# Optimization experiments

Measured on AMD Instinct MI355X. Metric: run time of the kernel, lower is better.

## Reference

```python
import jax, jax.numpy as jnp
import numpy as np

B, N, D = 2, 256, 512
H = 4 * D  # mlp_hidden_dim


def setup_inputs() -> dict:
    key = jax.random.key(0)
    ks = jax.random.split(key, 14)
    s_in = 1.0 / np.sqrt(D)
    s_h = 1.0 / np.sqrt(H)
    s_cat = 1.0 / np.sqrt(2 * D)
    return {
        "x_v": jax.random.normal(ks[0], (B, N, D), jnp.float32),
        "x_a": jax.random.normal(ks[1], (B, N, D), jnp.float32),
        # weights stored as (in, out); y = x @ W + b (same math as torch Linear)
        "W1v": jax.random.uniform(ks[2], (D, H), jnp.float32, -s_in, s_in),
        "b1v": jax.random.uniform(ks[3], (H,), jnp.float32, -s_in, s_in),
        "W1a": jax.random.uniform(ks[4], (D, H), jnp.float32, -s_in, s_in),
        "b1a": jax.random.uniform(ks[5], (H,), jnp.float32, -s_in, s_in),
        "Wmv": jax.random.uniform(ks[6], (H, D), jnp.float32, -s_h, s_h),
        "bmv": jax.random.uniform(ks[7], (D,), jnp.float32, -s_h, s_h),
        "Wma": jax.random.uniform(ks[8], (H, D), jnp.float32, -s_h, s_h),
        "bma": jax.random.uniform(ks[9], (D,), jnp.float32, -s_h, s_h),
        "Wout": jax.random.uniform(ks[10], (2 * D, D), jnp.float32, -s_cat, s_cat),
        "bout": jax.random.uniform(ks[11], (D,), jnp.float32, -s_cat, s_cat),
    }


def reference(x_v, x_a, W1v, b1v, W1a, b1a, Wmv, bmv, Wma, bma, Wout, bout):
    # pairwise Manhattan distance: [B, N, M]
    dist = jnp.sum(jnp.abs(x_v[:, :, None, :] - x_a[:, None, :, :]), axis=-1)
    dv = dist.mean(axis=2)  # [B, N] mean distance of each v-token to all a-tokens
    da = dist.mean(axis=1)  # [B, M]
    xv_w = x_v * dv[..., None]
    xa_w = x_a * da[..., None]
    # dropout prob = 0.0 -> identity
    hv = jax.nn.gelu(xv_w @ W1v + b1v, approximate=False) @ Wmv + bmv
    ha = jax.nn.gelu(xa_w @ W1a + b1a, approximate=False) @ Wma + bma
    combined = jnp.concatenate([hv, ha], axis=-1)  # [B, N, 2D]
    return combined @ Wout + bout
```

## Files before the change

kernel.cpp:

```cpp
#include <hip/hip_runtime.h>
#include <math.h>

#define Bsz  2
#define Ntok 256
#define Ddim 512
#define Hdim 2048
#define Mrows 512

typedef __bf16 bf16_8 __attribute__((ext_vector_type(8)));
typedef __bf16 bf16_4 __attribute__((ext_vector_type(4)));
typedef __bf16 bf16_2 __attribute__((ext_vector_type(2)));
typedef float  f32x4_t __attribute__((ext_vector_type(4)));

struct PrepPtrs {
    const float* src[3];
    __bf16*      dst[3];
    const float* xv;
    const float* xa;
    __bf16*      xbf[2];
    float*       pv;
    float*       pa;
    const float* bm[2];
    const float* Wout;
    const float* bout;
    float*       bc;
    float*       outz;
};

__global__ __launch_bounds__(256) void prep_kernel(PrepPtrs p) {
    __shared__ float tile[64][65];
    __shared__ float red[4][4];

    int blk = blockIdx.x;
    int tid = threadIdx.x;

    if (blk < 640) {
        const int Ks[3]  = {512, 512, 1024};
        const int Ns[3]  = {2048, 2048, 512};
        const int off[4] = {0, 256, 512, 640};
        int mi = 0;
        while (blk >= off[mi + 1]) ++mi;
        int local = blk - off[mi];
        int shift = (mi < 2) ? 5 : 3;
        int bx = local & ((1 << shift) - 1);
        int by = local >> shift;
        const float* src = p.src[mi];
        __bf16*      dst = p.dst[mi];
        int K = Ks[mi], N = Ns[mi];
        int n0 = bx << 6, k0 = by << 6;

        int klb = tid >> 4, nl = (tid & 15) << 2;
#pragma unroll
        for (int pass = 0; pass < 4; ++pass) {
            int kl = (pass << 4) + klb;
            float4 v = *(const float4*)&src[(size_t)(k0 + kl) * N + n0 + nl];
            tile[kl][nl + 0] = v.x;
            tile[kl][nl + 1] = v.y;
            tile[kl][nl + 2] = v.z;
            tile[kl][nl + 3] = v.w;
        }
        __syncthreads();
        int nl2 = tid >> 2, kb = (tid & 3) << 2;
#pragma unroll
        for (int pass = 0; pass < 4; ++pass) {
            int kl2 = (pass << 4) + kb;
            bf16_4 o;
#pragma unroll
            for (int i = 0; i < 4; ++i) o[i] = (__bf16)tile[kl2 + i][nl2];
            *(bf16_4*)&dst[(size_t)(n0 + nl2) * K + k0 + kl2] = o;
        }
    } else if (blk < 1664) {
        int bx   = blk - 640;
        int jc   = bx & 3;
        int g    = bx >> 2;
        int role = g >> 7;
        int b    = (g >> 6) & 1;
        int i0   = (g & 63) << 2;
        const float* Q    = role ? p.xa : p.xv;
        const float* S    = role ? p.xv : p.xa;
        float*       outp = role ? p.pa : p.pv;

        int d0 = tid << 1;
        const float* Qb = Q + ((size_t)b * Ntok + i0) * Ddim + d0;
        const float* Sb = S + ((size_t)b * Ntok + (jc << 6)) * Ddim + d0;

        float2 q[4];
#pragma unroll
        for (int r = 0; r < 4; ++r) q[r] = *(const float2*)(Qb + r * Ddim);

        if (jc == 0) {
            __bf16* xb = p.xbf[role];
#pragma unroll
            for (int r = 0; r < 4; ++r) {
                bf16_2 o;
                o[0] = (__bf16)q[r].x;
                o[1] = (__bf16)q[r].y;
                *(bf16_2*)&xb[((size_t)b * Ntok + i0 + r) * Ddim + d0] = o;
            }
        }

        float acc[4] = {0.f, 0.f, 0.f, 0.f};
#pragma unroll 4
        for (int j = 0; j < 64; ++j) {
            float2 s = *(const float2*)(Sb + (size_t)j * Ddim);
#pragma unroll
            for (int r = 0; r < 4; ++r)
                acc[r] += fabsf(q[r].x - s.x) + fabsf(q[r].y - s.y);
        }
        int lane = tid & 63, wv = tid >> 6;
#pragma unroll
        for (int r = 0; r < 4; ++r) {
            float v = acc[r];
#pragma unroll
            for (int off2 = 32; off2; off2 >>= 1) v += __shfl_down(v, off2);
            if (lane == 0) red[wv][r] = v;
        }
        __syncthreads();
        if (tid < 4) {
            float v = red[0][tid] + red[1][tid] + red[2][tid] + red[3][tid];
            outp[jc * Mrows + b * Ntok + i0 + tid] = v;
        }
    } else if (blk < 1672) {
        int kb = blk - 1664;
        float a0 = 0.f, a1 = 0.f, a2 = 0.f, a3 = 0.f;
#pragma unroll 4
        for (int kk = 0; kk < 128; kk += 2) {
            int k0 = (kb << 7) + kk, k1 = k0 + 1;
            float bk0 = (k0 < 512) ? p.bm[0][k0] : p.bm[1][k0 - 512];
            float bk1 = (k1 < 512) ? p.bm[0][k1] : p.bm[1][k1 - 512];
            a0 += bk0 * p.Wout[(size_t)k0 * Ddim + tid];
            a1 += bk0 * p.Wout[(size_t)k0 * Ddim + tid + 256];
            a2 += bk1 * p.Wout[(size_t)k1 * Ddim + tid];
            a3 += bk1 * p.Wout[(size_t)k1 * Ddim + tid + 256];
        }
        if (kb == 0) { a0 += p.bout[tid]; a1 += p.bout[tid + 256]; }
        p.bc[(kb << 9) + tid]       = a0 + a2;
        p.bc[(kb << 9) + tid + 256] = a1 + a3;
    } else {
        int ib = blk - 1672;
        float4 z4 = {0.f, 0.f, 0.f, 0.f};
        float4* o = (float4*)p.outz + (size_t)ib * 1024 + tid;
#pragma unroll
        for (int pass = 0; pass < 4; ++pass) o[pass * 256] = z4;
    }
}

template <int GELU, int AMODE, int BFP32, int OUTM>
__device__ void gemm_tile(__bf16 (&As)[2][64][40], __bf16 (&Bs)[2][128][40],
                          const void* Aa, int lda, const void* Bv, int ldb,
                          const float* bias, const float* scale4,
                          void* C, int ldc, int Kdim,
                          int m0, int n0, int addBias) {
    const int tid = threadIdx.x;
    const int arow = tid >> 2;
    const int akc  = (tid & 3) << 3;
    const int brow = tid >> 1;
    const int bkc  = (tid & 1) << 4;

    const __bf16* Ab = (const __bf16*)Aa + (size_t)(m0 + arow) * lda + akc;
    const float*  Af = (const float*) Aa + (size_t)(m0 + arow) * lda + akc;
    const __bf16* Bb = (const __bf16*)Bv + (size_t)(n0 + brow) * ldb + bkc;
    const float*  Bf = (const float*) Bv + (size_t)(n0 + brow) * ldb + bkc;

    float s = 1.0f;
    if (AMODE == 1 || AMODE == 3) {
        int m = m0 + arow;
        s = (scale4[m] + scale4[Mrows + m] + scale4[2 * Mrows + m] +
             scale4[3 * Mrows + m]) * (1.0f / 256.0f);
    }

    const int wave = tid >> 6, lane = tid & 63;
    const int moff = (wave >> 1) << 5;
    const int noff = (wave & 1) << 6;
    const int lrow = lane & 15, quad = lane >> 4;

    struct Stage {
        float4 aF0, aF1;
        float4 bF0, bF1, bF2, bF3;
        bf16_8 a8;
        bf16_8 b8a, b8b;
    };
    Stage sR, sN;

    auto loadStage = [&](int kt, Stage& st) {
        if (BFP32) {
            st.bF0 = *(const float4*)(Bf + kt);
            st.bF1 = *(const float4*)(Bf + kt + 4);
            st.bF2 = *(const float4*)(Bf + kt + 8);
            st.bF3 = *(const float4*)(Bf + kt + 12);
        } else {
            st.b8a = *(const bf16_8*)(Bb + kt);
            st.b8b = *(const bf16_8*)(Bb + kt + 8);
        }
        if (AMODE == 1) {
            st.aF0 = *(const float4*)(Af + kt);
            st.aF1 = *(const float4*)(Af + kt + 4);
        } else {
            st.a8 = *(const bf16_8*)(Ab + kt);
        }
    };
    auto storeStage = [&](int buf, const Stage& st) {
        bf16_8 a8;
        if (AMODE == 1) {
            a8[0] = (__bf16)(st.aF0.x * s); a8[1] = (__bf16)(st.aF0.y * s);
            a8[2] = (__bf16)(st.aF0.z * s); a8[3] = (__bf16)(st.aF0.w * s);
            a8[4] = (__bf16)(st.aF1.x * s); a8[5] = (__bf16)(st.aF1.y * s);
            a8[6] = (__bf16)(st.aF1.z * s); a8[7] = (__bf16)(st.aF1.w * s);
        } else if (AMODE == 3) {
#pragma unroll
            for (int i = 0; i < 8; ++i)
                a8[i] = (__bf16)((float)st.a8[i] * s);
        } else {
            a8 = st.a8;
        }
        bf16_8 b8a, b8b;
        if (BFP32) {
            b8a[0] = (__bf16)st.bF0.x; b8a[1] = (__bf16)st.bF0.y;
            b8a[2] = (__bf16)st.bF0.z; b8a[3] = (__bf16)st.bF0.w;
            b8a[4] = (__bf16)st.bF1.x; b8a[5] = (__bf16)st.bF1.y;
            b8a[6] = (__bf16)st.bF1.z; b8a[7] = (__bf16)st.bF1.w;
            b8b[0] = (__bf16)st.bF2.x; b8b[1] = (__bf16)st.bF2.y;
            b8b[2] = (__bf16)st.bF2.z; b8b[3] = (__bf16)st.bF2.w;
            b8b[4] = (__bf16)st.bF3.x; b8b[5] = (__bf16)st.bF3.y;
            b8b[6] = (__bf16)st.bF3.z; b8b[7] = (__bf16)st.bF3.w;
        } else {
            b8a = st.b8a;
            b8b = st.b8b;
        }
        *(bf16_8*)&As[buf][arow][akc] = a8;
        *(bf16_8*)&Bs[buf][brow][bkc]     = b8a;
        *(bf16_8*)&Bs[buf][brow][bkc + 8] = b8b;
    };

    f32x4_t acc0[4], acc1[4];
#pragma unroll
    for (int j = 0; j < 4; ++j) {
        acc0[j] = {0.f, 0.f, 0.f, 0.f};
        acc1[j] = {0.f, 0.f, 0.f, 0.f};
    }

    const int nIter = Kdim >> 5;

    loadStage(0, sR);
    storeStage(0, sR);
    if (nIter > 1) loadStage(32, sR);
    __syncthreads();

    for (int it = 0; it < nIter; ++it) {
        const int cur = it & 1;
        bf16_8 a0 = *(const bf16_8*)&As[cur][moff + lrow][quad << 3];
        bf16_8 a1 = *(const bf16_8*)&As[cur][moff + 16 + lrow][quad << 3];
        bf16_8 b[4];
#pragma unroll
        for (int j = 0; j < 4; ++j)
            b[j] = *(const bf16_8*)&Bs[cur][noff + (j << 4) + lrow][quad << 3];
        if (it + 2 < nIter) loadStage((it + 2) << 5, sN);
#pragma unroll
        for (int j = 0; j < 4; ++j) {
            acc0[j] = __builtin_amdgcn_mfma_f32_16x16x32_bf16(a0, b[j], acc0[j], 0, 0, 0);
            acc1[j] = __builtin_amdgcn_mfma_f32_16x16x32_bf16(a1, b[j], acc1[j], 0, 0, 0);
        }
        if (it + 1 < nIter) {
            storeStage(cur ^ 1, sR);
            sR = sN;
            __syncthreads();
        }
    }

#pragma unroll
    for (int ti = 0; ti < 2; ++ti) {
#pragma unroll
        for (int tj = 0; tj < 4; ++tj) {
            int colg = n0 + noff + (tj << 4) + lrow;
            float bv = 0.0f;
            if (addBias == 1) {
                bv = bias[colg];
            } else if (addBias == 2) {
#pragma unroll
                for (int k = 0; k < 8; ++k) bv += bias[(k << 9) + colg];
            }
            f32x4_t av = ti ? acc1[tj] : acc0[tj];
#pragma unroll
            for (int r = 0; r < 4; ++r) {
                int rowg = m0 + moff + (ti << 4) + (quad << 2) + r;
                float v = av[r] + bv;
                if (GELU) v = 0.5f * v * (1.0f + erff(v * 0.70710678118654752f));
                if (OUTM == 1)
                    ((__bf16*)C)[(size_t)rowg * ldc + colg] = (__bf16)v;
                else
                    atomicAdd((float*)C + (size_t)rowg * ldc + colg, v);
            }
        }
    }
}

struct APtrs {
    const __bf16* xbf[2];
    const __bf16* WT1[2];
    const float*  b1[2];
    const float*  pd[2];
    __bf16*       g1[2];
    const __bf16* WTout;
    const float*  Wm[2];
    __bf16*       WcT[2];
};

__global__ __launch_bounds__(256) void kernelA(APtrs p) {
    __shared__ __align__(16) __bf16 As[2][64][40];
    __shared__ __align__(16) __bf16 Bs[2][128][40];
    int blk = blockIdx.x;
    if (blk < 256) {
        int z = blk >> 7, t = blk & 127;
        int mt = t >> 4, nt = t & 15;
        gemm_tile<1, 3, 0, 1>(As, Bs, p.xbf[z], Ddim, p.WT1[z], Ddim,
                              p.b1[z], p.pd[z], p.g1[z], Hdim, Ddim,
                              mt << 6, nt << 7, 1);
    } else {
        int b2 = blk - 256;
        int z = b2 >> 7, t = b2 & 127;
        int mt = t >> 4, nt = t & 15;
        gemm_tile<0, 0, 1, 1>(As, Bs, p.WTout + z * 512, 2 * Ddim,
                              p.Wm[z], Ddim, nullptr, nullptr,
                              p.WcT[z], Hdim, Ddim, mt << 6, nt << 7, 0);
    }
}

struct BPtrs {
    const __bf16* g1[2];
    const __bf16* WcT[2];
    const float*  bc;
    float*        out;
};

__global__ __launch_bounds__(256) void kernelB(BPtrs p) {
    __shared__ __align__(16) __bf16 As[2][64][40];
    __shared__ __align__(16) __bf16 Bs[2][128][40];
    int nt = blockIdx.x & 3, mt = (blockIdx.x >> 2) & 7, kz = blockIdx.x >> 5;
    int z = kz >> 2, koff = (kz & 3) << 9;
    gemm_tile<0, 0, 0, 2>(As, Bs, p.g1[z] + koff, Hdim, p.WcT[z] + koff, Hdim,
                          p.bc, nullptr, p.out, Ddim, Ddim,
                          mt << 6, nt << 7, kz == 0 ? 2 : 0);
}

extern "C" void kernel_launch(void* const* d_in, const int* in_sizes, int n_in,
                              void* d_out, int out_size, void* d_ws, size_t ws_size,
                              hipStream_t stream) {
    const float* x_v  = (const float*)d_in[0];
    const float* x_a  = (const float*)d_in[1];
    const float* W1v  = (const float*)d_in[2];
    const float* b1v  = (const float*)d_in[3];
    const float* W1a  = (const float*)d_in[4];
    const float* b1a  = (const float*)d_in[5];
    const float* Wmv  = (const float*)d_in[6];
    const float* bmv  = (const float*)d_in[7];
    const float* Wma  = (const float*)d_in[8];
    const float* bma  = (const float*)d_in[9];
    const float* Wout = (const float*)d_in[10];
    const float* bout = (const float*)d_in[11];
    float* out = (float*)d_out;

    char* w = (char*)d_ws;
    auto alloc = [&](size_t bytes) {
        char* r = w;
        w += (bytes + 255) & ~(size_t)255;
        return (void*)r;
    };
    float*    pv    = (float*)alloc(4 * Mrows * 4);
    float*    pa    = (float*)alloc(4 * Mrows * 4);
    float*    bc    = (float*)alloc(8 * Ddim * 4);
    __bf16*   xbfv  = (__bf16*)alloc((size_t)Mrows * Ddim * 2);
    __bf16*   xbfa  = (__bf16*)alloc((size_t)Mrows * Ddim * 2);
    __bf16*   WT1v  = (__bf16*)alloc((size_t)Hdim * Ddim * 2);
    __bf16*   WT1a  = (__bf16*)alloc((size_t)Hdim * Ddim * 2);
    __bf16*   WTout = (__bf16*)alloc((size_t)Ddim * 2 * Ddim * 2);
    __bf16*   WcTv  = (__bf16*)alloc((size_t)Ddim * Hdim * 2);
    __bf16*   WcTa  = (__bf16*)alloc((size_t)Ddim * Hdim * 2);
    __bf16*   g1v   = (__bf16*)alloc((size_t)Mrows * Hdim * 2);
    __bf16*   g1a   = (__bf16*)alloc((size_t)Mrows * Hdim * 2);

    PrepPtrs pp;
    pp.src[0] = W1v;  pp.dst[0] = WT1v;
    pp.src[1] = W1a;  pp.dst[1] = WT1a;
    pp.src[2] = Wout; pp.dst[2] = WTout;
    pp.xv = x_v; pp.xa = x_a;
    pp.xbf[0] = xbfv; pp.xbf[1] = xbfa;
    pp.pv = pv; pp.pa = pa;
    pp.bm[0] = bmv; pp.bm[1] = bma;
    pp.Wout = Wout; pp.bout = bout;
    pp.bc = bc;
    pp.outz = out;
    prep_kernel<<<dim3(1736), dim3(256), 0, stream>>>(pp);

    APtrs ap;
    ap.xbf[0] = xbfv; ap.xbf[1] = xbfa;
    ap.WT1[0] = WT1v; ap.WT1[1] = WT1a;
    ap.b1[0] = b1v; ap.b1[1] = b1a;
    ap.pd[0] = pv; ap.pd[1] = pa;
    ap.g1[0] = g1v; ap.g1[1] = g1a;
    ap.WTout = WTout;
    ap.Wm[0] = Wmv; ap.Wm[1] = Wma;
    ap.WcT[0] = WcTv; ap.WcT[1] = WcTa;
    kernelA<<<dim3(512), dim3(256), 0, stream>>>(ap);

    BPtrs bp;
    bp.g1[0] = g1v; bp.g1[1] = g1a;
    bp.WcT[0] = WcTv; bp.WcT[1] = WcTa;
    bp.bc = bc; bp.out = out;
    kernelB<<<dim3(256), dim3(256), 0, stream>>>(bp);
}
```

Baseline: 131.7 us.

## Fuse prep and two GEMM kernels into one cooperative persistent kernel

```diff
diff --git a/kernel.cpp b/kernel.cpp
--- a/kernel.cpp
+++ b/kernel.cpp
@@ -1,5 +1,8 @@
 #include <hip/hip_runtime.h>
+#include <hip/hip_cooperative_groups.h>
 #include <math.h>
+
+namespace cg = cooperative_groups;
 
 #define Bsz  2
 #define Ntok 256
@@ -12,7 +15,12 @@
 typedef __bf16 bf16_2 __attribute__((ext_vector_type(2)));
 typedef float  f32x4_t __attribute__((ext_vector_type(4)));
 
-struct PrepPtrs {
+union __align__(16) SharedU {
+    struct { float tile[64][65]; float red[4][4]; } pr;
+    struct { __bf16 As[2][64][40]; __bf16 Bs[2][128][40]; } gm;
+};
+
+struct FusedPtrs {
     const float* src[3];
     __bf16*      dst[3];
     const float* xv;
@@ -24,16 +32,16 @@
     const float* Wout;
     const float* bout;
     float*       bc;
-    float*       outz;
+    const float* b1[2];
+    const float* Wm[2];
+    const __bf16* WT1[2];
+    const __bf16* WTout;
+    __bf16*      WcT[2];
+    __bf16*      g1[2];
+    float*       out;
 };
 
-__global__ __launch_bounds__(256) void prep_kernel(PrepPtrs p) {
-    __shared__ float tile[64][65];
-    __shared__ float red[4][4];
-
-    int blk = blockIdx.x;
-    int tid = threadIdx.x;
-
+__device__ void prep_job(int blk, int tid, const FusedPtrs& p, SharedU& sh) {
     if (blk < 640) {
         const int Ks[3]  = {512, 512, 1024};
         const int Ns[3]  = {2048, 2048, 512};
@@ -54,10 +62,10 @@
         for (int pass = 0; pass < 4; ++pass) {
             int kl = (pass << 4) + klb;
             float4 v = *(const float4*)&src[(size_t)(k0 + kl) * N + n0 + nl];
-            tile[kl][nl + 0] = v.x;
-            tile[kl][nl + 1] = v.y;
-            tile[kl][nl + 2] = v.z;
-            tile[kl][nl + 3] = v.w;
+            sh.pr.tile[kl][nl + 0] = v.x;
+            sh.pr.tile[kl][nl + 1] = v.y;
+            sh.pr.tile[kl][nl + 2] = v.z;
+            sh.pr.tile[kl][nl + 3] = v.w;
         }
         __syncthreads();
         int nl2 = tid >> 2, kb = (tid & 3) << 2;
@@ -66,7 +74,7 @@
             int kl2 = (pass << 4) + kb;
             bf16_4 o;
 #pragma unroll
-            for (int i = 0; i < 4; ++i) o[i] = (__bf16)tile[kl2 + i][nl2];
+            for (int i = 0; i < 4; ++i) o[i] = (__bf16)sh.pr.tile[kl2 + i][nl2];
             *(bf16_4*)&dst[(size_t)(n0 + nl2) * K + k0 + kl2] = o;
         }
     } else if (blk < 1664) {
@@ -113,11 +121,12 @@
             float v = acc[r];
 #pragma unroll
             for (int off2 = 32; off2; off2 >>= 1) v += __shfl_down(v, off2);
-            if (lane == 0) red[wv][r] = v;
+            if (lane == 0) sh.pr.red[wv][r] = v;
         }
         __syncthreads();
         if (tid < 4) {
-            float v = red[0][tid] + red[1][tid] + red[2][tid] + red[3][tid];
+            float v = sh.pr.red[0][tid] + sh.pr.red[1][tid] +
+                      sh.pr.red[2][tid] + sh.pr.red[3][tid];
             outp[jc * Mrows + b * Ntok + i0 + tid] = v;
         }
     } else if (blk < 1672) {
@@ -139,7 +148,7 @@
     } else {
         int ib = blk - 1672;
         float4 z4 = {0.f, 0.f, 0.f, 0.f};
-        float4* o = (float4*)p.outz + (size_t)ib * 1024 + tid;
+        float4* o = (float4*)p.out + (size_t)ib * 1024 + tid;
 #pragma unroll
         for (int pass = 0; pass < 4; ++pass) o[pass * 256] = z4;
     }
@@ -294,52 +303,45 @@
     }
 }
 
-struct APtrs {
-    const __bf16* xbf[2];
-    const __bf16* WT1[2];
-    const float*  b1[2];
-    const float*  pd[2];
-    __bf16*       g1[2];
-    const __bf16* WTout;
-    const float*  Wm[2];
-    __bf16*       WcT[2];
-};
-
-__global__ __launch_bounds__(256) void kernelA(APtrs p) {
-    __shared__ __align__(16) __bf16 As[2][64][40];
-    __shared__ __align__(16) __bf16 Bs[2][128][40];
-    int blk = blockIdx.x;
-    if (blk < 256) {
-        int z = blk >> 7, t = blk & 127;
-        int mt = t >> 4, nt = t & 15;
-        gemm_tile<1, 3, 0, 1>(As, Bs, p.xbf[z], Ddim, p.WT1[z], Ddim,
-                              p.b1[z], p.pd[z], p.g1[z], Hdim, Ddim,
-                              mt << 6, nt << 7, 1);
-    } else {
-        int b2 = blk - 256;
-        int z = b2 >> 7, t = b2 & 127;
-        int mt = t >> 4, nt = t & 15;
-        gemm_tile<0, 0, 1, 1>(As, Bs, p.WTout + z * 512, 2 * Ddim,
-                              p.Wm[z], Ddim, nullptr, nullptr,
-                              p.WcT[z], Hdim, Ddim, mt << 6, nt << 7, 0);
-    }
-}
-
-struct BPtrs {
-    const __bf16* g1[2];
-    const __bf16* WcT[2];
-    const float*  bc;
-    float*        out;
-};
-
-__global__ __launch_bounds__(256) void kernelB(BPtrs p) {
-    __shared__ __align__(16) __bf16 As[2][64][40];
-    __shared__ __align__(16) __bf16 Bs[2][128][40];
-    int nt = blockIdx.x & 3, mt = (blockIdx.x >> 2) & 7, kz = blockIdx.x >> 5;
-    int z = kz >> 2, koff = (kz & 3) << 9;
-    gemm_tile<0, 0, 0, 2>(As, Bs, p.g1[z] + koff, Hdim, p.WcT[z] + koff, Hdim,
-                          p.bc, nullptr, p.out, Ddim, Ddim,
-                          mt << 6, nt << 7, kz == 0 ? 2 : 0);
+__global__ __launch_bounds__(256, 2) void fused_kernel(FusedPtrs p) {
+    __shared__ SharedU sh;
+    const int tid = threadIdx.x;
+    cg::grid_group grid = cg::this_grid();
+
+    for (int j = blockIdx.x; j < 1736; j += 512) {
+        prep_job(j, tid, p, sh);
+        __syncthreads();
+    }
+    grid.sync();
+
+    {
+        int blk = blockIdx.x;
+        if (blk < 256) {
+            int z = blk >> 7, t = blk & 127;
+            int mt = t >> 4, nt = t & 15;
+            gemm_tile<1, 3, 0, 1>(sh.gm.As, sh.gm.Bs, p.xbf[z], Ddim,
+                                  p.WT1[z], Ddim, p.b1[z],
+                                  z ? p.pa : p.pv, p.g1[z], Hdim, Ddim,
+                                  mt << 6, nt << 7, 1);
+        } else {
+            int b2 = blk - 256;
+            int z = b2 >> 7, t = b2 & 127;
+            int mt = t >> 4, nt = t & 15;
+            gemm_tile<0, 0, 1, 1>(sh.gm.As, sh.gm.Bs, p.WTout + z * 512,
+                                  2 * Ddim, p.Wm[z], Ddim, nullptr, nullptr,
+                                  p.WcT[z], Hdim, Ddim, mt << 6, nt << 7, 0);
+        }
+    }
+    grid.sync();
+
+    if (blockIdx.x < 256) {
+        int nt = blockIdx.x & 3, mt = (blockIdx.x >> 2) & 7, kz = blockIdx.x >> 5;
+        int z = kz >> 2, koff = (kz & 3) << 9;
+        gemm_tile<0, 0, 0, 2>(sh.gm.As, sh.gm.Bs, p.g1[z] + koff, Hdim,
+                              p.WcT[z] + koff, Hdim, p.bc, nullptr,
+                              p.out, Ddim, Ddim,
+                              mt << 6, nt << 7, kz == 0 ? 2 : 0);
+    }
 }
 
 extern "C" void kernel_launch(void* const* d_in, const int* in_sizes, int n_in,
@@ -378,33 +380,25 @@
     __bf16*   g1v   = (__bf16*)alloc((size_t)Mrows * Hdim * 2);
     __bf16*   g1a   = (__bf16*)alloc((size_t)Mrows * Hdim * 2);
 
-    PrepPtrs pp;
-    pp.src[0] = W1v;  pp.dst[0] = WT1v;
-    pp.src[1] = W1a;  pp.dst[1] = WT1a;
-    pp.src[2] = Wout; pp.dst[2] = WTout;
-    pp.xv = x_v; pp.xa = x_a;
-    pp.xbf[0] = xbfv; pp.xbf[1] = xbfa;
-    pp.pv = pv; pp.pa = pa;
-    pp.bm[0] = bmv; pp.bm[1] = bma;
-    pp.Wout = Wout; pp.bout = bout;
-    pp.bc = bc;
-    pp.outz = out;
-    prep_kernel<<<dim3(1736), dim3(256), 0, stream>>>(pp);
-
-    APtrs ap;
-    ap.xbf[0] = xbfv; ap.xbf[1] = xbfa;
-    ap.WT1[0] = WT1v; ap.WT1[1] = WT1a;
-    ap.b1[0] = b1v; ap.b1[1] = b1a;
-    ap.pd[0] = pv; ap.pd[1] = pa;
-    ap.g1[0] = g1v; ap.g1[1] = g1a;
-    ap.WTout = WTout;
-    ap.Wm[0] = Wmv; ap.Wm[1] = Wma;
-    ap.WcT[0] = WcTv; ap.WcT[1] = WcTa;
-    kernelA<<<dim3(512), dim3(256), 0, stream>>>(ap);
-
-    BPtrs bp;
-    bp.g1[0] = g1v; bp.g1[1] = g1a;
-    bp.WcT[0] = WcTv; bp.WcT[1] = WcTa;
-    bp.bc = bc; bp.out = out;
-    kernelB<<<dim3(256), dim3(256), 0, stream>>>(bp);
+    FusedPtrs fp;
+    fp.src[0] = W1v;  fp.dst[0] = WT1v;
+    fp.src[1] = W1a;  fp.dst[1] = WT1a;
+    fp.src[2] = Wout; fp.dst[2] = WTout;
+    fp.xv = x_v; fp.xa = x_a;
+    fp.xbf[0] = xbfv; fp.xbf[1] = xbfa;
+    fp.pv = pv; fp.pa = pa;
+    fp.bm[0] = bmv; fp.bm[1] = bma;
+    fp.Wout = Wout; fp.bout = bout;
+    fp.bc = bc;
+    fp.b1[0] = b1v; fp.b1[1] = b1a;
+    fp.Wm[0] = Wmv; fp.Wm[1] = Wma;
+    fp.WT1[0] = WT1v; fp.WT1[1] = WT1a;
+    fp.WTout = WTout;
+    fp.WcT[0] = WcTv; fp.WcT[1] = WcTa;
+    fp.g1[0] = g1v; fp.g1[1] = g1a;
+    fp.out = out;
+
+    void* args[] = { (void*)&fp };
+    hipLaunchCooperativeKernel((const void*)fused_kernel, dim3(512), dim3(256),
+                               args, 0, stream);
 }
```

Result: slower. 283.0 us (+114.9%).
